# Optimization experiments

Measured on AMD Instinct MI355X. Metric: run time of the kernel, lower is better.

Reference implementation:

```python
import jax, jax.numpy as jnp
import numpy as np

K = 3
TAU = 1.0
EPS = 1e-8


def _route_dense(z, k, tau):
    """RouterTopK forward -> dense combine weights [N, L].
    Matches torch: topk values, softmax(topv/tau). Softmax is permutation
    invariant so sorted top_k gives identical math to sorted=False."""
    topi = jax.lax.top_k(z, k)[1]                      # [N, k] int32
    topv = jnp.take_along_axis(z, topi, axis=1)        # [N, k]
    w = jax.nn.softmax(topv / (tau + EPS), axis=1)     # [N, k]
    N, L = z.shape
    dw = jnp.zeros((N, L), z.dtype)
    dw = dw.at[jnp.arange(N)[:, None], topi].add(w)
    return dw


def _apply_mixture(x, dw, W):
    """y[n] = sum_e dw[n,e] * (W[e] @ x[n]).  Loop over the small fixed
    expert count (12); equivalent math to the sort+grouped-GEMM dispatch."""
    y = jnp.zeros((x.shape[0], W.shape[1]), x.dtype)
    for e in range(W.shape[0]):
        y = y + (x @ W[e].T) * dw[:, e:e + 1]
    return y


def setup_inputs() -> dict:
    key = jax.random.key(0)
    ks = jax.random.split(key, 8)
    B, T, D_in, H, D_out, L, d_addr = 4, 2048, 1024, 4096, 1024, 12, 64

    def unitize(U):
        U = U - U.mean(axis=1, keepdims=True)
        return U / (jnp.linalg.norm(U, axis=1, keepdims=True) + EPS)

    x = jax.random.normal(ks[0], (B, T, D_in), jnp.float32)
    P_w = jax.random.normal(ks[1], (d_addr, D_in), jnp.float32) / np.sqrt(D_in)
    U1 = unitize(jax.random.normal(ks[2], (L, d_addr), jnp.float32))
    U2 = unitize(jax.random.normal(ks[3], (L, d_addr), jnp.float32))
    U3 = unitize(jax.random.normal(ks[4], (L, d_addr), jnp.float32))
    W1 = jax.random.normal(ks[5], (L, H, D_in), jnp.float32)
    W1 = W1 / jnp.linalg.norm(W1.reshape(L, -1), axis=1)[:, None, None]
    W2 = jax.random.normal(ks[6], (L, D_out, H), jnp.float32)
    W2 = W2 / jnp.linalg.norm(W2.reshape(L, -1), axis=1)[:, None, None]
    b2 = jax.random.normal(ks[7], (L, D_out), jnp.float32)
    b2 = b2 / jnp.linalg.norm(b2, axis=1, keepdims=True)
    return {"x": x, "P_w": P_w, "U1": U1, "U2": U2, "U3": U3,
            "W1": W1, "W2": W2, "b2": b2}


def reference(x, P_w, U1, U2, U3, W1, W2, b2):
    B, T, D = x.shape
    x_flat = x.reshape(B * T, D)                       # [N, D_in]
    x_addr = x_flat @ P_w.T                            # [N, d_addr]
    dw1 = _route_dense(x_addr @ U1.T, K, TAU)          # [N, L]
    dw2 = _route_dense(x_addr @ U2.T, K, TAU)
    dw3 = _route_dense(x_addr @ U3.T, K, TAU)
    h = _apply_mixture(x_flat, dw1, W1)                # [N, H]
    h = jax.nn.gelu(h, approximate=False)              # nn.GELU (exact)
    y = _apply_mixture(h, dw2, W2)                     # [N, D_out]
    y = y + dw3 @ b2                                   # grouped bias add
    return y.reshape(B, T, -1)
```

## Files before the change

kernel.cpp:

```cpp
#include <hip/hip_runtime.h>
#include <math.h>

#define DEVI __device__ __forceinline__
typedef unsigned short u16;
typedef unsigned int u32;
typedef unsigned char u8;
typedef float f32x4 __attribute__((ext_vector_type(4)));
typedef float fx4 __attribute__((ext_vector_type(4)));
typedef u32 ux4 __attribute__((ext_vector_type(4)));
typedef long lx2 __attribute__((ext_vector_type(2)));

static constexpr int CAP = 8192;

DEVI u16 f2b(float f) {
  u32 x = __builtin_bit_cast(u32, f);
  u32 r = (x + 0x7fffu + ((x >> 16) & 1u)) >> 16;
  return (u16)r;
}
DEVI float b2f(u16 u) { return __builtin_bit_cast(float, (u32)u << 16); }

DEVI u32 f2fp8(float f) {
  u32 x = __builtin_bit_cast(u32, f);
  u32 s = (x >> 24) & 0x80u;
  u32 ax = x & 0x7fffffffu;
  if (ax >= 0x43e80000u) return s | 0x7eu;
  if (ax < 0x3a800000u) return s;
  if (ax < 0x3c800000u) {
    float m = __builtin_bit_cast(float, ax) * 512.0f;
    return s | (u32)rintf(m);
  }
  u32 r = ax + 0x7ffffu + ((ax >> 20) & 1u);
  return s | (((r >> 23) - 120u) << 3) | ((r >> 20) & 7u);
}

#if __has_builtin(__builtin_amdgcn_cvt_pk_fp8_f32)
DEVI u32 pack4hw(float a, float b, float c, float d, float sc) {
  u32 lo = __builtin_amdgcn_cvt_pk_fp8_f32(a * sc, b * sc, 0, false);
  return (u32)__builtin_amdgcn_cvt_pk_fp8_f32(c * sc, d * sc, lo, true);
}
#else
DEVI u32 pack4hw(float a, float b, float c, float d, float sc) {
  return f2fp8(a * sc) | (f2fp8(b * sc) << 8) | (f2fp8(c * sc) << 16) | (f2fp8(d * sc) << 24);
}
#endif

DEVI void async16(const void* g, void* l) {
  __builtin_amdgcn_global_load_lds((const __attribute__((address_space(1))) void*)g,
                                   (__attribute__((address_space(3))) void*)l, 16, 0, 0);
}

__global__ void cvt8_k(const float* __restrict__ s0, u8* __restrict__ d0,
                       const float* __restrict__ s1, u8* __restrict__ d1, long n) {
  long nq0 = n / 4, nq = nq0 * 2;
  long stride = (long)gridDim.x * blockDim.x;
  for (long q = (long)blockIdx.x * blockDim.x + threadIdx.x; q < nq; q += stride) {
    long qi = q; const float* s = s0; u8* d = d0;
    if (qi >= nq0) { qi -= nq0; s = s1; d = d1; }
    fx4 v = __builtin_nontemporal_load((const fx4*)s + qi);
    u32 o = pack4hw(v.x, v.y, v.z, v.w, 1024.f);
    long b = qi >> 4; int s4 = (int)(qi & 15); int g = s4 >> 1;
    *(u32*)(d + b * 64 + 16 * (g & 3) + 8 * (g >> 2) + 4 * (s4 & 1)) = o;
  }
}

__global__ __launch_bounds__(256) void xaddr2_k(
    const float* __restrict__ x, const float* __restrict__ Pw,
    double* __restrict__ xa_g, u8* __restrict__ xb) {
  __shared__ __align__(16) char sm[19584];
  float* xs  = (float*)sm;
  float* pws = (float*)(sm + 2176);

  const int tid = threadIdx.x;
  const int tok0 = blockIdx.x * 8;
  const int kbase = blockIdx.y * 512;
  const int tok = tid >> 5, dg = tid & 31;

  double a0 = 0, a1 = 0, a2 = 0, a3 = 0;

  const int rot0 = dg >> 3;
  const int rot1 = (dg >> 3) + 4;

  for (int kc = 0; kc < 8; ++kc) {
    const int k0 = kbase + kc * 64;
    if (tid < 128) {
      int t = tid >> 4, c4 = tid & 15;
      size_t goff = (size_t)(tok0 + t) * 1024 + k0 + c4 * 4;
      fx4 v = __builtin_nontemporal_load((const fx4*)&x[goff]);
      *(fx4*)&xs[t * 68 + c4 * 4] = v;
      int g = c4 >> 1;
      int off = 16 * (g & 3) + 8 * (g >> 2) + 4 * (c4 & 1);
      u32 o8 = pack4hw(v.x, v.y, v.z, v.w, 1.0f);
      *(u32*)&xb[(size_t)(tok0 + t) * 1024 + k0 + off] = o8;
    }
#pragma unroll
    for (int j = 0; j < 4; ++j) {
      int f = tid + 256 * j;
      int pr = f >> 4, pc = f & 15;
      int pos = (pc + (pr >> 3)) & 15;
      *(float4*)&pws[pr * 68 + pos * 4] = *(const float4*)&Pw[(size_t)pr * 1024 + k0 + pc * 4];
    }
    __syncthreads();
    const float* xrow = &xs[tok * 68];
#pragma unroll
    for (int k4 = 0; k4 < 16; ++k4) {
      float4 xv = *(const float4*)&xrow[k4 * 4];
      float4 q0 = *(const float4*)&pws[dg * 68 + ((k4 + rot0) & 15) * 4];
      float4 q1 = *(const float4*)&pws[(dg + 32) * 68 + ((k4 + rot1) & 15) * 4];
      a0 += (double)xv.x * q0.x + (double)xv.y * q0.y;
      a1 += (double)xv.z * q0.z + (double)xv.w * q0.w;
      a2 += (double)xv.x * q1.x + (double)xv.y * q1.y;
      a3 += (double)xv.z * q1.z + (double)xv.w * q1.w;
    }
    __syncthreads();
  }

  size_t base = ((size_t)blockIdx.y * 8192 + (tok0 + tok)) * 64;
  xa_g[base + dg] = a0 + a1;
  xa_g[base + dg + 32] = a2 + a3;
}

__global__ __launch_bounds__(256) void route2_k(
    const double* __restrict__ xa_g,
    const float* __restrict__ U1, const float* __restrict__ U2, const float* __restrict__ U3,
    const float* __restrict__ b2,
    int* __restrict__ cnt, int* __restrict__ ltok, float* __restrict__ lwgt,
    float* __restrict__ out) {
  __shared__ double xa[16][66];
  __shared__ float us[36][68];
  __shared__ double zz[16][40];
  __shared__ int se[16][4];
  __shared__ float swg[16][4];

  const int tid = threadIdx.x;
  const int tok0 = blockIdx.x * 16;

  {
    const int tk = tid >> 4, j = tid & 15;
    const double* s0 = &xa_g[(size_t)(tok0 + tk) * 64 + j * 4];
    const double* s1 = s0 + (size_t)8192 * 64;
#pragma unroll
    for (int m = 0; m < 4; ++m) xa[tk][j * 4 + m] = s0[m] + s1[m];
  }
  if (tid < 144) {
#pragma unroll
    for (int j = 0; j < 4; ++j) {
      int f = tid * 4 + j;
      int r = f >> 4, c4 = f & 15;
      const float* U = (r < 12) ? (U1 + r * 64) : (r < 24 ? U2 + (r - 12) * 64 : U3 + (r - 24) * 64);
      *(float4*)&us[r][c4 * 4] = *(const float4*)&U[c4 * 4];
    }
  }
  __syncthreads();

#pragma unroll
  for (int rep = 0; rep < 3; ++rep) {
    int idx = tid + 256 * rep;
    if (idx < 576) {
      int tk = idx / 36, re = idx - tk * 36;
      double acc = 0;
      const double* xr = &xa[tk][0];
      const float* ur = &us[re][0];
      for (int k = 0; k < 64; ++k) acc += xr[k] * (double)ur[k];
      zz[tk][re] = acc;
    }
  }
  __syncthreads();

  if (tid < 48) {
    const int tk = tid & 15, r = tid >> 4;
    const double* z = &zz[tk][r * 12];
    double v0 = -1e300, v1 = -1e300, v2 = -1e300;
    int i0 = 0, i1 = 0, i2 = 0;
    for (int e = 0; e < 12; ++e) {
      double v = z[e];
      if (v > v0)      { v2 = v1; i2 = i1; v1 = v0; i1 = i0; v0 = v; i0 = e; }
      else if (v > v1) { v2 = v1; i2 = i1; v1 = v; i1 = e; }
      else if (v > v2) { v2 = v; i2 = e; }
    }
    const double inv_tau = 1.0 / (1.0 + 1e-8);
    double e1 = exp((v1 - v0) * inv_tau), e2 = exp((v2 - v0) * inv_tau);
    double s = 1.0 / (1.0 + e1 + e2);
    double w0 = s, w1 = e1 * s, w2 = e2 * s;
    int n = tok0 + tk;
    if (r < 2) {
      int jj3[3] = { i0, i1, i2 };
      double ww[3] = { w0, w1, w2 };
      for (int j = 0; j < 3; ++j) {
        int slot = (r * 3 + j) * 12 + jj3[j];
        int pos = atomicAdd(&cnt[slot], 1);
        ltok[slot * CAP + pos] = n;
        lwgt[slot * CAP + pos] = (float)ww[j];
      }
    } else {
      se[tk][0] = i0; se[tk][1] = i1; se[tk][2] = i2;
      swg[tk][0] = (float)w0; swg[tk][1] = (float)w1; swg[tk][2] = (float)w2;
    }
  }
  __syncthreads();

#pragma unroll
  for (int j = 0; j < 16; ++j) {
    int f = tid + 256 * j;
    int tk = f >> 8, c4 = f & 255;
    const float w0 = swg[tk][0], w1 = swg[tk][1], w2 = swg[tk][2];
    float4 a = *(const float4*)&b2[(size_t)se[tk][0] * 1024 + c4 * 4];
    float4 b = *(const float4*)&b2[(size_t)se[tk][1] * 1024 + c4 * 4];
    float4 d = *(const float4*)&b2[(size_t)se[tk][2] * 1024 + c4 * 4];
    fx4 o;
    o.x = w0 * a.x + w1 * b.x + w2 * d.x;
    o.y = w0 * a.y + w1 * b.y + w2 * d.y;
    o.z = w0 * a.z + w1 * b.z + w2 * d.z;
    o.w = w0 * a.w + w1 * b.w + w2 * d.w;
    __builtin_nontemporal_store(o, (fx4*)&out[(size_t)(tok0 + tk) * 1024 + c4 * 4]);
  }
}

__global__ void build_k(const int* __restrict__ cnt, int2* __restrict__ desc,
                        int* __restrict__ ntl) {
  int t = threadIdx.x;
  if (t < 6) {
    int nt = 0;
    for (int e = 0; e < 12; ++e) {
      int c = cnt[t * 12 + e];
      for (int s = 0; s < c; s += 128) { desc[t * 96 + nt] = make_int2(e, s); ++nt; }
    }
    ntl[t] = nt;
  }
}

template<int KB, int NOUT, bool ADD, typename CT>
__global__ __launch_bounds__(256, 4) void moe_gemm(
    const u8* __restrict__ A, const u8* __restrict__ W, CT* __restrict__ C,
    float outScale,
    const int* __restrict__ cnt12, const int* __restrict__ ltok12,
    const float* __restrict__ lwgt12,
    const int2* __restrict__ desc, const int* __restrict__ ntl) {
  unsigned lin = blockIdx.y * gridDim.x + blockIdx.x;
  unsigned q = (gridDim.x * gridDim.y) >> 3;
  unsigned swz = (lin & 7) * q + (lin >> 3);
  int tile = swz % gridDim.x;
  int ntile = swz / gridDim.x;
  if (tile >= *ntl) return;
  const int2 dd = desc[tile];
  const int e = dd.x, rowStart = dd.y;
  const int rows = min(128, cnt12[e] - rowStart);
  const int base = e * CAP + rowStart;

  __shared__ __align__(16) u8 As[2][8192];
  __shared__ __align__(16) u8 Bs[2][8192];
  __shared__ int tokL[128];
  __shared__ float wgtL[128];

  const int tid = threadIdx.x;
  const int lane = tid & 63, w = tid >> 6;
  if (tid < 128) {
    int li = min(tid, rows - 1);
    tokL[tid] = ltok12[base + li];
    wgtL[tid] = lwgt12[base + li];
  }
  __syncthreads();

  const int srcSwz = (((tid & 3) ^ ((tid >> 3) & 3)) * 16);
  const u8* aSrc[2]; const u8* bSrc[2];
#pragma unroll
  for (int i = 0; i < 2; ++i) {
    int r = i * 64 + (tid >> 2);
    aSrc[i] = A + (size_t)tokL[min(r, rows - 1)] * KB + srcSwz;
    bSrc[i] = W + ((size_t)e * NOUT + ntile * 128 + r) * KB + srcSwz;
  }

  f32x4 acc[4][4] = {};
  const int wr = w >> 1, wc = w & 1;
  const int roff = 16 * ((((lane >> 4) & 3)) ^ ((lane >> 1) & 3));
  constexpr int NT = KB / 64;

#define STAGE(kt_) do { int ko_ = (kt_) * 64; int b_ = (kt_) & 1;               \
    async16(aSrc[0] + ko_, &As[b_][tid * 16]);                                  \
    async16(aSrc[1] + ko_, &As[b_][(256 + tid) * 16]);                          \
    async16(bSrc[0] + ko_, &Bs[b_][tid * 16]);                                  \
    async16(bSrc[1] + ko_, &Bs[b_][(256 + tid) * 16]); } while (0)

  STAGE(0);
  __syncthreads();
  for (int kt = 0; kt < NT; ++kt) {
    if (kt + 1 < NT) STAGE(kt + 1);
    const u8* Ab = &As[kt & 1][0];
    const u8* Bb = &Bs[kt & 1][0];
    lx2 bv[4], av[4];
#pragma unroll
    for (int ni = 0; ni < 4; ++ni) {
      int rB = wc * 64 + ni * 16 + (lane & 15);
      bv[ni] = *(const lx2*)&Bb[rB * 64 + roff];
    }
#pragma unroll
    for (int mi = 0; mi < 4; ++mi) {
      int rA = wr * 64 + mi * 16 + (lane & 15);
      av[mi] = *(const lx2*)&Ab[rA * 64 + roff];
    }
#pragma unroll
    for (int mi = 0; mi < 4; ++mi)
#pragma unroll
      for (int ni = 0; ni < 4; ++ni)
        acc[mi][ni] = __builtin_amdgcn_mfma_f32_16x16x32_fp8_fp8(av[mi].x, bv[ni].x, acc[mi][ni], 0, 0, 0);
#pragma unroll
    for (int mi = 0; mi < 4; ++mi)
#pragma unroll
      for (int ni = 0; ni < 4; ++ni)
        acc[mi][ni] = __builtin_amdgcn_mfma_f32_16x16x32_fp8_fp8(av[mi].y, bv[ni].y, acc[mi][ni], 0, 0, 0);
    __syncthreads();
  }
#undef STAGE

#pragma unroll
  for (int mi = 0; mi < 4; ++mi) {
    int lr0 = wr * 64 + mi * 16 + ((lane >> 4) << 2);
#pragma unroll
    for (int rr = 0; rr < 4; ++rr) {
      int lrow = lr0 + rr;
      bool rowok = lrow < rows;
      int tok = tokL[lrow];
      float wv = wgtL[lrow] * outScale;
      if constexpr (sizeof(CT) == 2) {
        u32* cp32 = (u32*)((u16*)C + (size_t)tok * NOUT + ntile * 128 + wc * 64 + (lane & 14));
#pragma unroll
        for (int ni = 0; ni < 4; ++ni) {
          float v = acc[mi][ni][rr] * wv;
          float vo = __shfl_xor(v, 1);
          if (rowok && !(lane & 1)) {
            float lo = v, hi = vo;
            if (ADD) {
              u32 curv = __builtin_nontemporal_load(cp32 + ni * 8);
              lo += b2f((u16)(curv & 0xffffu));
              hi += b2f((u16)(curv >> 16));
            }
            __builtin_nontemporal_store((u32)f2b(lo) | ((u32)f2b(hi) << 16), cp32 + ni * 8);
          }
        }
      } else {
        if (rowok) {
          float* cp = (float*)C + (size_t)tok * NOUT + ntile * 128 + wc * 64 + (lane & 15);
#pragma unroll
          for (int ni = 0; ni < 4; ++ni) {
            float val = acc[mi][ni][rr] * wv;
            float* p = cp + ni * 16;
            float res = ADD ? (__builtin_nontemporal_load(p) + val) : val;
            __builtin_nontemporal_store(res, p);
          }
        }
      }
    }
  }
}

DEVI float gelu1(float v) { return 0.5f * v * (1.0f + erff(v * 0.70710678118654752f)); }
__global__ void gelu8_k(const u32* __restrict__ h, u8* __restrict__ h8, long n8) {
  long stride = (long)gridDim.x * blockDim.x;
  const ux4* hp = (const ux4*)h;
  for (long i = (long)blockIdx.x * blockDim.x + threadIdx.x; i < n8; i += stride) {
    ux4 v = __builtin_nontemporal_load(hp + i);
    u32 words[4] = { v.x, v.y, v.z, v.w };
    float gf[8];
#pragma unroll
    for (int j = 0; j < 4; ++j) {
      gf[2 * j]     = gelu1(b2f((u16)(words[j] & 0xffffu)));
      gf[2 * j + 1] = gelu1(b2f((u16)(words[j] >> 16)));
    }
    u32 lo = pack4hw(gf[0], gf[1], gf[2], gf[3], 256.f);
    u32 hi = pack4hw(gf[4], gf[5], gf[6], gf[7], 256.f);
    long b = i >> 3; int g = (int)(i & 7);
    u32* dst = (u32*)(h8 + b * 64 + 16 * (g & 3) + 8 * (g >> 2));
    dst[0] = lo; dst[1] = hi;
  }
}

extern "C" void kernel_launch(void* const* d_in, const int* in_sizes, int n_in,
                              void* d_out, int out_size, void* d_ws, size_t ws_size,
                              hipStream_t stream) {
  const float* x  = (const float*)d_in[0];
  const float* Pw = (const float*)d_in[1];
  const float* U1 = (const float*)d_in[2];
  const float* U2 = (const float*)d_in[3];
  const float* U3 = (const float*)d_in[4];
  const float* W1 = (const float*)d_in[5];
  const float* W2 = (const float*)d_in[6];
  const float* b2 = (const float*)d_in[7];
  float* out = (float*)d_out;

  char* ws = (char*)d_ws;
  size_t o = 0;
  u8*  W1b = (u8*)(ws + o); o += (size_t)12 * 4096 * 1024;
  u8*  W2b = (u8*)(ws + o); o += (size_t)12 * 1024 * 4096;
  u8*  xb  = (u8*)(ws + o); o += (size_t)8192 * 1024;
  u16* h   = (u16*)(ws + o); o += (size_t)8192 * 4096 * 2;
  u8*  h8  = (u8*)(ws + o); o += (size_t)8192 * 4096;
  double* xa_g = (double*)(ws + o); o += (size_t)2 * 8192 * 64 * 8;
  int* cnt = (int*)(ws + o); o += 512;
  int2* desc = (int2*)(ws + o); o += (size_t)6 * 96 * sizeof(int2);
  o = (o + 255) & ~(size_t)255;
  int* ntl = (int*)(ws + o); o += 256;
  int* ltok = (int*)(ws + o); o += (size_t)6 * 12 * CAP * 4;
  float* lwgt = (float*)(ws + o); o += (size_t)6 * 12 * CAP * 4;
  if (ws_size < o) return;

  hipMemsetAsync(cnt, 0, 512, stream);
  cvt8_k<<<4096, 256, 0, stream>>>(W1, W1b, W2, W2b, (long)12 * 4096 * 1024);
  xaddr2_k<<<dim3(1024, 2), 256, 0, stream>>>(x, Pw, xa_g, xb);
  route2_k<<<512, 256, 0, stream>>>(xa_g, U1, U2, U3, b2, cnt, ltok, lwgt, out);
  build_k<<<1, 64, 0, stream>>>(cnt, desc, ntl);

  const float s1 = 1.0f / 1024.f;
  const float s2 = 1.0f / (1024.f * 256.f);

  {
    dim3 g(80, 32);
    int s;
    s = 0; moe_gemm<1024, 4096, false, u16><<<g, 256, 0, stream>>>(xb, W1b, h, s1, cnt + s * 12, ltok + (size_t)s * 12 * CAP, lwgt + (size_t)s * 12 * CAP, desc + s * 96, ntl + s);
    s = 1; moe_gemm<1024, 4096, true , u16><<<g, 256, 0, stream>>>(xb, W1b, h, s1, cnt + s * 12, ltok + (size_t)s * 12 * CAP, lwgt + (size_t)s * 12 * CAP, desc + s * 96, ntl + s);
    s = 2; moe_gemm<1024, 4096, true , u16><<<g, 256, 0, stream>>>(xb, W1b, h, s1, cnt + s * 12, ltok + (size_t)s * 12 * CAP, lwgt + (size_t)s * 12 * CAP, desc + s * 96, ntl + s);
  }

  gelu8_k<<<2048, 256, 0, stream>>>((const u32*)h, h8, (long)8192 * 4096 / 8);

  {
    dim3 g(80, 8);
    int s;
    s = 3; moe_gemm<4096, 1024, true, float><<<g, 256, 0, stream>>>(h8, W2b, out, s2, cnt + s * 12, ltok + (size_t)s * 12 * CAP, lwgt + (size_t)s * 12 * CAP, desc + s * 96, ntl + s);
    s = 4; moe_gemm<4096, 1024, true, float><<<g, 256, 0, stream>>>(h8, W2b, out, s2, cnt + s * 12, ltok + (size_t)s * 12 * CAP, lwgt + (size_t)s * 12 * CAP, desc + s * 96, ntl + s);
    s = 5; moe_gemm<4096, 1024, true, float><<<g, 256, 0, stream>>>(h8, W2b, out, s2, cnt + s * 12, ltok + (size_t)s * 12 * CAP, lwgt + (size_t)s * 12 * CAP, desc + s * 96, ntl + s);
  }
}
```

Measured before the change: 1.037 ms.

## Fuse GELU and fp8 quantization into last up-projection GEMM epilogue

New measurement: 884.5 us. 14.7% less time.

```diff
diff --git a/kernel.cpp b/kernel.cpp
--- a/kernel.cpp
+++ b/kernel.cpp
@@ -8,7 +8,6 @@
 typedef float f32x4 __attribute__((ext_vector_type(4)));
 typedef float fx4 __attribute__((ext_vector_type(4)));
 typedef u32 ux4 __attribute__((ext_vector_type(4)));
-typedef long lx2 __attribute__((ext_vector_type(2)));
 
 static constexpr int CAP = 8192;
 
@@ -38,16 +37,24 @@
   u32 lo = __builtin_amdgcn_cvt_pk_fp8_f32(a * sc, b * sc, 0, false);
   return (u32)__builtin_amdgcn_cvt_pk_fp8_f32(c * sc, d * sc, lo, true);
 }
+DEVI u32 pack2hw(float a, float b, float sc) {
+  return __builtin_amdgcn_cvt_pk_fp8_f32(a * sc, b * sc, 0, false) & 0xffffu;
+}
 #else
 DEVI u32 pack4hw(float a, float b, float c, float d, float sc) {
   return f2fp8(a * sc) | (f2fp8(b * sc) << 8) | (f2fp8(c * sc) << 16) | (f2fp8(d * sc) << 24);
 }
+DEVI u32 pack2hw(float a, float b, float sc) {
+  return f2fp8(a * sc) | (f2fp8(b * sc) << 8);
+}
 #endif
 
 DEVI void async16(const void* g, void* l) {
   __builtin_amdgcn_global_load_lds((const __attribute__((address_space(1))) void*)g,
                                    (__attribute__((address_space(3))) void*)l, 16, 0, 0);
 }
+
+DEVI float gelu1(float v) { return 0.5f * v * (1.0f + erff(v * 0.70710678118654752f)); }
 
 __global__ void cvt8_k(const float* __restrict__ s0, u8* __restrict__ d0,
                        const float* __restrict__ s1, u8* __restrict__ d1, long n) {
@@ -57,9 +64,7 @@
     long qi = q; const float* s = s0; u8* d = d0;
     if (qi >= nq0) { qi -= nq0; s = s1; d = d1; }
     fx4 v = __builtin_nontemporal_load((const fx4*)s + qi);
-    u32 o = pack4hw(v.x, v.y, v.z, v.w, 1024.f);
-    long b = qi >> 4; int s4 = (int)(qi & 15); int g = s4 >> 1;
-    *(u32*)(d + b * 64 + 16 * (g & 3) + 8 * (g >> 2) + 4 * (s4 & 1)) = o;
+    ((u32*)d)[qi] = pack4hw(v.x, v.y, v.z, v.w, 1024.f);
   }
 }
 
@@ -87,10 +92,7 @@
       size_t goff = (size_t)(tok0 + t) * 1024 + k0 + c4 * 4;
       fx4 v = __builtin_nontemporal_load((const fx4*)&x[goff]);
       *(fx4*)&xs[t * 68 + c4 * 4] = v;
-      int g = c4 >> 1;
-      int off = 16 * (g & 3) + 8 * (g >> 2) + 4 * (c4 & 1);
-      u32 o8 = pack4hw(v.x, v.y, v.z, v.w, 1.0f);
-      *(u32*)&xb[(size_t)(tok0 + t) * 1024 + k0 + off] = o8;
+      *(u32*)&xb[goff] = pack4hw(v.x, v.y, v.z, v.w, 1.0f);
     }
 #pragma unroll
     for (int j = 0; j < 4; ++j) {
@@ -206,12 +208,12 @@
     float4 a = *(const float4*)&b2[(size_t)se[tk][0] * 1024 + c4 * 4];
     float4 b = *(const float4*)&b2[(size_t)se[tk][1] * 1024 + c4 * 4];
     float4 d = *(const float4*)&b2[(size_t)se[tk][2] * 1024 + c4 * 4];
-    fx4 o;
+    float4 o;
     o.x = w0 * a.x + w1 * b.x + w2 * d.x;
     o.y = w0 * a.y + w1 * b.y + w2 * d.y;
     o.z = w0 * a.z + w1 * b.z + w2 * d.z;
     o.w = w0 * a.w + w1 * b.w + w2 * d.w;
-    __builtin_nontemporal_store(o, (fx4*)&out[(size_t)(tok0 + tk) * 1024 + c4 * 4]);
+    *(float4*)&out[(size_t)(tok0 + tk) * 1024 + c4 * 4] = o;
   }
 }
 
@@ -228,10 +230,10 @@
   }
 }
 
-template<int KB, int NOUT, bool ADD, typename CT>
+template<int KB, int NOUT, bool ADD, bool GELU, typename CT>
 __global__ __launch_bounds__(256, 4) void moe_gemm(
     const u8* __restrict__ A, const u8* __restrict__ W, CT* __restrict__ C,
-    float outScale,
+    u8* __restrict__ h8o, float outScale,
     const int* __restrict__ cnt12, const int* __restrict__ ltok12,
     const float* __restrict__ lwgt12,
     const int2* __restrict__ desc, const int* __restrict__ ntl) {
@@ -271,7 +273,10 @@
 
   f32x4 acc[4][4] = {};
   const int wr = w >> 1, wc = w & 1;
-  const int roff = 16 * ((((lane >> 4) & 3)) ^ ((lane >> 1) & 3));
+  const int sxr = (lane >> 1) & 3;
+  const int p8 = ((lane >> 4) & 1) * 8;
+  const int roff0 = 16 * (((lane >> 5) | 0) ^ sxr) + p8;
+  const int roff1 = 16 * (((lane >> 5) | 2) ^ sxr) + p8;
   constexpr int NT = KB / 64;
 
 #define STAGE(kt_) do { int ko_ = (kt_) * 64; int b_ = (kt_) & 1;               \
@@ -286,27 +291,24 @@
     if (kt + 1 < NT) STAGE(kt + 1);
     const u8* Ab = &As[kt & 1][0];
     const u8* Bb = &Bs[kt & 1][0];
-    lx2 bv[4], av[4];
-#pragma unroll
-    for (int ni = 0; ni < 4; ++ni) {
-      int rB = wc * 64 + ni * 16 + (lane & 15);
-      bv[ni] = *(const lx2*)&Bb[rB * 64 + roff];
-    }
-#pragma unroll
-    for (int mi = 0; mi < 4; ++mi) {
-      int rA = wr * 64 + mi * 16 + (lane & 15);
-      av[mi] = *(const lx2*)&Ab[rA * 64 + roff];
-    }
-#pragma unroll
-    for (int mi = 0; mi < 4; ++mi)
-#pragma unroll
-      for (int ni = 0; ni < 4; ++ni)
-        acc[mi][ni] = __builtin_amdgcn_mfma_f32_16x16x32_fp8_fp8(av[mi].x, bv[ni].x, acc[mi][ni], 0, 0, 0);
-#pragma unroll
-    for (int mi = 0; mi < 4; ++mi)
-#pragma unroll
-      for (int ni = 0; ni < 4; ++ni)
-        acc[mi][ni] = __builtin_amdgcn_mfma_f32_16x16x32_fp8_fp8(av[mi].y, bv[ni].y, acc[mi][ni], 0, 0, 0);
+#pragma unroll
+    for (int kk = 0; kk < 2; ++kk) {
+      const int ro = kk ? roff1 : roff0;
+      long bf[4];
+#pragma unroll
+      for (int ni = 0; ni < 4; ++ni) {
+        int rB = wc * 64 + ni * 16 + (lane & 15);
+        bf[ni] = *(const long*)&Bb[rB * 64 + ro];
+      }
+#pragma unroll
+      for (int mi = 0; mi < 4; ++mi) {
+        int rA = wr * 64 + mi * 16 + (lane & 15);
+        long af = *(const long*)&Ab[rA * 64 + ro];
+#pragma unroll
+        for (int ni = 0; ni < 4; ++ni)
+          acc[mi][ni] = __builtin_amdgcn_mfma_f32_16x16x32_fp8_fp8(af, bf[ni], acc[mi][ni], 0, 0, 0);
+      }
+    }
     __syncthreads();
   }
 #undef STAGE
@@ -321,7 +323,8 @@
       int tok = tokL[lrow];
       float wv = wgtL[lrow] * outScale;
       if constexpr (sizeof(CT) == 2) {
-        u32* cp32 = (u32*)((u16*)C + (size_t)tok * NOUT + ntile * 128 + wc * 64 + (lane & 14));
+        size_t celt = (size_t)tok * NOUT + ntile * 128 + wc * 64 + (lane & 14);
+        u32* cp32 = (u32*)((u16*)C + celt);
 #pragma unroll
         for (int ni = 0; ni < 4; ++ni) {
           float v = acc[mi][ni][rr] * wv;
@@ -329,11 +332,16 @@
           if (rowok && !(lane & 1)) {
             float lo = v, hi = vo;
             if (ADD) {
-              u32 curv = __builtin_nontemporal_load(cp32 + ni * 8);
+              u32 curv = cp32[ni * 8];
               lo += b2f((u16)(curv & 0xffffu));
               hi += b2f((u16)(curv >> 16));
             }
-            __builtin_nontemporal_store((u32)f2b(lo) | ((u32)f2b(hi) << 16), cp32 + ni * 8);
+            if constexpr (GELU) {
+              *(u16*)(h8o + celt + ni * 16) =
+                  (u16)pack2hw(gelu1(lo), gelu1(hi), 256.f);
+            } else {
+              cp32[ni * 8] = (u32)f2b(lo) | ((u32)f2b(hi) << 16);
+            }
           }
         }
       } else {
@@ -343,33 +351,11 @@
           for (int ni = 0; ni < 4; ++ni) {
             float val = acc[mi][ni][rr] * wv;
             float* p = cp + ni * 16;
-            float res = ADD ? (__builtin_nontemporal_load(p) + val) : val;
-            __builtin_nontemporal_store(res, p);
+            *p = ADD ? (*p + val) : val;
           }
         }
       }
     }
-  }
-}
-
-DEVI float gelu1(float v) { return 0.5f * v * (1.0f + erff(v * 0.70710678118654752f)); }
-__global__ void gelu8_k(const u32* __restrict__ h, u8* __restrict__ h8, long n8) {
-  long stride = (long)gridDim.x * blockDim.x;
-  const ux4* hp = (const ux4*)h;
-  for (long i = (long)blockIdx.x * blockDim.x + threadIdx.x; i < n8; i += stride) {
-    ux4 v = __builtin_nontemporal_load(hp + i);
-    u32 words[4] = { v.x, v.y, v.z, v.w };
-    float gf[8];
-#pragma unroll
-    for (int j = 0; j < 4; ++j) {
-      gf[2 * j]     = gelu1(b2f((u16)(words[j] & 0xffffu)));
-      gf[2 * j + 1] = gelu1(b2f((u16)(words[j] >> 16)));
-    }
-    u32 lo = pack4hw(gf[0], gf[1], gf[2], gf[3], 256.f);
-    u32 hi = pack4hw(gf[4], gf[5], gf[6], gf[7], 256.f);
-    long b = i >> 3; int g = (int)(i & 7);
-    u32* dst = (u32*)(h8 + b * 64 + 16 * (g & 3) + 8 * (g >> 2));
-    dst[0] = lo; dst[1] = hi;
   }
 }
 
@@ -414,18 +400,16 @@
   {
     dim3 g(80, 32);
     int s;
-    s = 0; moe_gemm<1024, 4096, false, u16><<<g, 256, 0, stream>>>(xb, W1b, h, s1, cnt + s * 12, ltok + (size_t)s * 12 * CAP, lwgt + (size_t)s * 12 * CAP, desc + s * 96, ntl + s);
-    s = 1; moe_gemm<1024, 4096, true , u16><<<g, 256, 0, stream>>>(xb, W1b, h, s1, cnt + s * 12, ltok + (size_t)s * 12 * CAP, lwgt + (size_t)s * 12 * CAP, desc + s * 96, ntl + s);
-    s = 2; moe_gemm<1024, 4096, true , u16><<<g, 256, 0, stream>>>(xb, W1b, h, s1, cnt + s * 12, ltok + (size_t)s * 12 * CAP, lwgt + (size_t)s * 12 * CAP, desc + s * 96, ntl + s);
-  }
-
-  gelu8_k<<<2048, 256, 0, stream>>>((const u32*)h, h8, (long)8192 * 4096 / 8);
+    s = 0; moe_gemm<1024, 4096, false, false, u16><<<g, 256, 0, stream>>>(xb, W1b, h, h8, s1, cnt + s * 12, ltok + (size_t)s * 12 * CAP, lwgt + (size_t)s * 12 * CAP, desc + s * 96, ntl + s);
+    s = 1; moe_gemm<1024, 4096, true , false, u16><<<g, 256, 0, stream>>>(xb, W1b, h, h8, s1, cnt + s * 12, ltok + (size_t)s * 12 * CAP, lwgt + (size_t)s * 12 * CAP, desc + s * 96, ntl + s);
+    s = 2; moe_gemm<1024, 4096, true , true , u16><<<g, 256, 0, stream>>>(xb, W1b, h, h8, s1, cnt + s * 12, ltok + (size_t)s * 12 * CAP, lwgt + (size_t)s * 12 * CAP, desc + s * 96, ntl + s);
+  }
 
   {
     dim3 g(80, 8);
     int s;
-    s = 3; moe_gemm<4096, 1024, true, float><<<g, 256, 0, stream>>>(h8, W2b, out, s2, cnt + s * 12, ltok + (size_t)s * 12 * CAP, lwgt + (size_t)s * 12 * CAP, desc + s * 96, ntl + s);
-    s = 4; moe_gemm<4096, 1024, true, float><<<g, 256, 0, stream>>>(h8, W2b, out, s2, cnt + s * 12, ltok + (size_t)s * 12 * CAP, lwgt + (size_t)s * 12 * CAP, desc + s * 96, ntl + s);
-    s = 5; moe_gemm<4096, 1024, true, float><<<g, 256, 0, stream>>>(h8, W2b, out, s2, cnt + s * 12, ltok + (size_t)s * 12 * CAP, lwgt + (size_t)s * 12 * CAP, desc + s * 96, ntl + s);
-  }
-}
+    s = 3; moe_gemm<4096, 1024, true, false, float><<<g, 256, 0, stream>>>(h8, W2b, out, nullptr, s2, cnt + s * 12, ltok + (size_t)s * 12 * CAP, lwgt + (size_t)s * 12 * CAP, desc + s * 96, ntl + s);
+    s = 4; moe_gemm<4096, 1024, true, false, float><<<g, 256, 0, stream>>>(h8, W2b, out, nullptr, s2, cnt + s * 12, ltok + (size_t)s * 12 * CAP, lwgt + (size_t)s * 12 * CAP, desc + s * 96, ntl + s);
+    s = 5; moe_gemm<4096, 1024, true, false, float><<<g, 256, 0, stream>>>(h8, W2b, out, nullptr, s2, cnt + s * 12, ltok + (size_t)s * 12 * CAP, lwgt + (size_t)s * 12 * CAP, desc + s * 96, ntl + s);
+  }
+}
```
